# Optimization experiments

Measured on AMD Instinct MI355X. Metric: run time of the kernel, lower is better.

Reference implementation:

```python
import jax, jax.numpy as jnp
import numpy as np

N, E, CIN, COUT = 50000, 800000, 64, 64
K_MAIN, K_SC = 5, 1
EPS = 1e-15      # PyG GMMConv sigma epsilon
BN_EPS = 1e-5    # BatchNorm epsilon


def gmm_conv(x, src, dst, pseudo, g, mu, sigma, root, bias):
    """PyG GMMConv with aggr='mean', root_weight=True, bias=True.
    x: [N,Cin], pseudo: [E,dim], g: [Cin,K*Cout], mu/sigma: [K,dim],
    root: [Cin,Cout], bias: [Cout]."""
    K = mu.shape[0]
    Cout = root.shape[1]
    n = x.shape[0]
    # Gaussian mixture weights per edge: [E,K]
    diff = pseudo[:, None, :] - mu[None, :, :]                     # [E,K,dim]
    gauss = jnp.exp((-0.5 * diff * diff / (EPS + sigma[None] ** 2)).sum(-1))
    # Project node features once at node level, then gather per edge
    xp = (x @ g).reshape(n, K, Cout)                               # [N,K,Cout]
    msg = jnp.einsum('ek,ekc->ec', gauss, xp[src])                 # [E,Cout]
    agg = jax.ops.segment_sum(msg, dst, num_segments=n)            # [N,Cout]
    deg = jax.ops.segment_sum(jnp.ones((src.shape[0],), x.dtype), dst,
                              num_segments=n)
    agg = agg / jnp.clip(deg, 1.0)[:, None]                        # mean aggr
    return agg + x @ root + bias


def batch_norm(x, gamma, beta):
    # SyncBatchNorm in training mode: batch stats over the node dimension
    m = x.mean(0)
    v = x.var(0)  # biased variance, as torch uses for normalization
    return (x - m) * jax.lax.rsqrt(v + BN_EPS) * gamma + beta


def _gmm_params(key, cin, cout, k):
    k1, k2, k3, k4 = jax.random.split(key, 4)
    scale = 1.0 / np.sqrt(cin)
    g = jax.random.normal(k1, (cin, k * cout), jnp.float32) * scale
    mu = jax.random.uniform(k2, (k, 1), jnp.float32)
    sigma = 1.0 + 0.1 * jax.random.uniform(k3, (k, 1), jnp.float32)
    root = jax.random.normal(k4, (cin, cout), jnp.float32) * scale
    bias = jnp.zeros((cout,), jnp.float32)
    return g, mu, sigma, root, bias


def setup_inputs() -> dict:
    key = jax.random.key(0)
    ks = jax.random.split(key, 8)
    x = jax.random.normal(ks[0], (N, CIN), jnp.float32)
    edge_index = jax.random.randint(ks[1], (2, E), 0, N, jnp.int64)
    edge_attr = jax.random.uniform(ks[2], (E, 1), jnp.float32)
    g1, mu1, sig1, root1, b1 = _gmm_params(ks[3], CIN, COUT, K_MAIN)
    g2, mu2, sig2, root2, b2 = _gmm_params(ks[4], COUT, COUT, K_MAIN)
    gs, mus, sigs, roots, bs = _gmm_params(ks[5], CIN, COUT, K_SC)
    ones = jnp.ones((COUT,), jnp.float32)
    zeros = jnp.zeros((COUT,), jnp.float32)
    return {
        'x': x, 'edge_index': edge_index, 'edge_attr': edge_attr,
        'g1': g1, 'mu1': mu1, 'sig1': sig1, 'root1': root1, 'b1': b1,
        'gam1': ones, 'bet1': zeros,
        'g2': g2, 'mu2': mu2, 'sig2': sig2, 'root2': root2, 'b2': b2,
        'gam2': ones, 'bet2': zeros,
        'gs': gs, 'mus': mus, 'sigs': sigs, 'roots': roots, 'bs': bs,
        'gams': ones, 'bets': zeros,
    }


def reference(x, edge_index, edge_attr,
              g1, mu1, sig1, root1, b1, gam1, bet1,
              g2, mu2, sig2, root2, b2, gam2, bet2,
              gs, mus, sigs, roots, bs, gams, bets):
    src, dst = edge_index[0], edge_index[1]
    h = gmm_conv(x, src, dst, edge_attr, g1, mu1, sig1, root1, b1)
    h = jax.nn.elu(batch_norm(h, gam1, bet1))
    h = gmm_conv(h, src, dst, edge_attr, g2, mu2, sig2, root2, b2)
    h = batch_norm(h, gam2, bet2)
    sc = gmm_conv(x, src, dst, edge_attr, gs, mus, sigs, roots, bs)
    sc = batch_norm(sc, gams, bets)
    return jax.nn.elu(h + sc)
```

## Files before the change

### kernel.cpp

```cpp
#include <hip/hip_runtime.h>
#include <hip/hip_bf16.h>


#define EPS_SIGMA 1e-15f
#define BN_EPS    1e-5f
#define PAD       48

typedef unsigned short ushortT;
typedef unsigned int uintT;
typedef __attribute__((ext_vector_type(8))) short bf16x8;
typedef __attribute__((ext_vector_type(4))) float f32x4;
typedef __attribute__((ext_vector_type(2))) float f32x2;

__device__ __forceinline__ ushortT f2bf(float f) {
  uintT b = __float_as_uint(f);
  b += 0x7FFFu + ((b >> 16) & 1u);
  return (ushortT)(b >> 16);
}
__device__ __forceinline__ float bf2f(ushortT u) {
  return __uint_as_float(((uintT)u) << 16);
}
__device__ __forceinline__ uintT pk2(float a, float b) {
  return (uintT)f2bf(a) | ((uintT)f2bf(b) << 16);
}

__device__ __forceinline__ void prep_one(const float* __restrict__ g,
                                         const float* __restrict__ root,
                                         ushortT* __restrict__ Bm, int K, int t) {
  int ks = t >> 8, rem = t & 255;
  int nt = rem >> 6, lane = rem & 63;
  int kbase = ks * 32 + (lane >> 4) * 8;
  int col = nt * 16 + (lane & 15);
  ushortT o[8];
#pragma unroll
  for (int j = 0; j < 8; ++j) {
    int r = kbase + j;
    float v;
    if (r < K * 64) {
      int k = r >> 6, i = r & 63;
      v = g[(size_t)i * (K * 64) + k * 64 + col];
    } else {
      v = root[(size_t)(r - K * 64) * 64 + col];
    }
    o[j] = f2bf(v);
  }
  *(uint4*)&Bm[(size_t)t * 8] = *(const uint4*)o;
}

__global__ void prologue(const float* __restrict__ x, ushortT* __restrict__ x_bf,
                         int total, int* __restrict__ cnt, float* __restrict__ stats,
                         int n, const void* ei, int* flag,
                         const float* g1, const float* root1, ushortT* Bm1,
                         const float* g2, const float* root2, ushortT* Bm2,
                         const float* gs, const float* roots, ushortT* Bmsc) {
  int t = blockIdx.x * 256 + threadIdx.x;
  int idx = t * 4;
  if (idx + 3 < total) {
    float4 v = *(const float4*)&x[idx];
    ushortT o[4] = {f2bf(v.x), f2bf(v.y), f2bf(v.z), f2bf(v.w)};
    *(uint2*)&x_bf[idx] = *(const uint2*)o;
  }
  if (t < n) cnt[t] = 0;
  if (t < 12 * 64) stats[t] = 0.f;
  if (blockIdx.x < 12) prep_one(g1, root1, Bm1, 5, t);
  else if (blockIdx.x < 24) prep_one(g2, root2, Bm2, 5, t - 12 * 256);
  else if (blockIdx.x < 28) prep_one(gs, roots, Bmsc, 1, t - 24 * 256);
  else if (blockIdx.x == 28) {
    const int* p = (const int*)ei;
    __shared__ int bad;
    if (threadIdx.x == 0) bad = 0;
    __syncthreads();
    if (p[threadIdx.x * 2 + 1] != 0) atomicAdd(&bad, 1);
    __syncthreads();
    if (threadIdx.x == 0) *flag = (bad == 0);
  }
}

__device__ __forceinline__ int load_idx(const void* ei, size_t pos, int is64) {
  if (is64) return (int)((const long long*)ei)[pos];
  return ((const int*)ei)[pos];
}

__global__ __launch_bounds__(256) void scatter_wgt(
    const void* ei, const float* __restrict__ ea, int E, const int* flag,
    int* __restrict__ cnt,
    const float* __restrict__ mu1, const float* __restrict__ sig1,
    const float* __restrict__ mus, const float* __restrict__ sigs,
    const float* __restrict__ mu2, const float* __restrict__ sig2,
    uint4* __restrict__ wbufC) {
  int e = blockIdx.x * 256 + threadIdx.x;
  if (e >= E) return;
  int is64 = *flag;
  int s = load_idx(ei, (size_t)e, is64);
  int d = load_idx(ei, (size_t)E + e, is64);
  float p = ea[e];
  int pos = atomicAdd(&cnt[d], 1);
  float w1[6], w2[5];
#pragma unroll
  for (int k = 0; k < 5; ++k) {
    float sg = sig1[k], df = p - mu1[k];
    w1[k] = __expf(-0.5f / (EPS_SIGMA + sg * sg) * df * df);
  }
  {
    float sg = sigs[0], df = p - mus[0];
    w1[5] = __expf(-0.5f / (EPS_SIGMA + sg * sg) * df * df);
  }
#pragma unroll
  for (int k = 0; k < 5; ++k) {
    float sg = sig2[k], df = p - mu2[k];
    w2[k] = __expf(-0.5f / (EPS_SIGMA + sg * sg) * df * df);
  }
  if (pos < PAD) {
    size_t slot = (size_t)d * PAD + pos;
    wbufC[slot * 2 + 0] = make_uint4(pk2(w1[0], w1[1]), pk2(w1[2], w1[3]),
                                     pk2(w1[4], w1[5]), (uintT)s);
    wbufC[slot * 2 + 1] = make_uint4(pk2(w2[0], w2[1]), pk2(w2[2], w2[3]),
                                     pk2(w2[4], 0.f), (uintT)s);
  }
}

template <int KT>
__device__ __forceinline__ void q_fma(f32x2* acc, uint4 r, uint2 xv) {
  f32x2 xlo, xhi;
  xlo.x = bf2f((ushortT)(xv.x & 0xffffu));
  xlo.y = bf2f((ushortT)(xv.x >> 16));
  xhi.x = bf2f((ushortT)(xv.y & 0xffffu));
  xhi.y = bf2f((ushortT)(xv.y >> 16));
  float w;
  f32x2 wv;
  w = bf2f((ushortT)(r.x & 0xffffu));
  wv.x = w; wv.y = w;
  acc[0] = __builtin_elementwise_fma(wv, xlo, acc[0]);
  acc[1] = __builtin_elementwise_fma(wv, xhi, acc[1]);
  if (KT > 1) {
    w = bf2f((ushortT)(r.x >> 16));
    wv.x = w; wv.y = w;
    acc[2] = __builtin_elementwise_fma(wv, xlo, acc[2]);
    acc[3] = __builtin_elementwise_fma(wv, xhi, acc[3]);
  }
  if (KT > 2) {
    w = bf2f((ushortT)(r.y & 0xffffu));
    wv.x = w; wv.y = w;
    acc[4] = __builtin_elementwise_fma(wv, xlo, acc[4]);
    acc[5] = __builtin_elementwise_fma(wv, xhi, acc[5]);
  }
  if (KT > 3) {
    w = bf2f((ushortT)(r.y >> 16));
    wv.x = w; wv.y = w;
    acc[6] = __builtin_elementwise_fma(wv, xlo, acc[6]);
    acc[7] = __builtin_elementwise_fma(wv, xhi, acc[7]);
  }
  if (KT > 4) {
    w = bf2f((ushortT)(r.z & 0xffffu));
    wv.x = w; wv.y = w;
    acc[8] = __builtin_elementwise_fma(wv, xlo, acc[8]);
    acc[9] = __builtin_elementwise_fma(wv, xhi, acc[9]);
  }
  if (KT > 5) {
    w = bf2f((ushortT)(r.z >> 16));
    wv.x = w; wv.y = w;
    acc[10] = __builtin_elementwise_fma(wv, xlo, acc[10]);
    acc[11] = __builtin_elementwise_fma(wv, xhi, acc[11]);
  }
}

template <int KT>
__global__ __launch_bounds__(256) void agg_pre(const ushortT* __restrict__ feat,
                                               const int* __restrict__ cnt,
                                               const uint4* __restrict__ wbufC, int off,
                                               ushortT* __restrict__ out, int n, int ldo) {
  int lane = threadIdx.x & 63;
  int q = lane >> 4;
  int c4 = lane & 15;
  int node = (blockIdx.x * 4 + (threadIdx.x >> 6)) * 4 + q;
  bool act = node < n;
  int deg = act ? cnt[node] : 0;
  int cap = deg < PAD ? deg : PAD;
  int beg = node * PAD;
  int end = beg + cap;
  f32x2 acc[2 * KT];
#pragma unroll
  for (int k = 0; k < 2 * KT; ++k) acc[k] = (f32x2){0.f, 0.f};
  int i = beg;
  for (; i + 4 <= end; i += 4) {
    uint4 r0 = wbufC[(size_t)(i + 0) * 2 + off];
    uint4 r1 = wbufC[(size_t)(i + 1) * 2 + off];
    uint4 r2 = wbufC[(size_t)(i + 2) * 2 + off];
    uint4 r3 = wbufC[(size_t)(i + 3) * 2 + off];
    uint2 x0 = *(const uint2*)&feat[((size_t)r0.w << 6) + c4 * 4];
    uint2 x1 = *(const uint2*)&feat[((size_t)r1.w << 6) + c4 * 4];
    uint2 x2 = *(const uint2*)&feat[((size_t)r2.w << 6) + c4 * 4];
    uint2 x3 = *(const uint2*)&feat[((size_t)r3.w << 6) + c4 * 4];
    q_fma<KT>(acc, r0, x0);
    q_fma<KT>(acc, r1, x1);
    q_fma<KT>(acc, r2, x2);
    q_fma<KT>(acc, r3, x3);
  }
  for (; i < end; ++i) {
    uint4 r = wbufC[(size_t)i * 2 + off];
    uint2 xv = *(const uint2*)&feat[((size_t)r.w << 6) + c4 * 4];
    q_fma<KT>(acc, r, xv);
  }
  if (act) {
    float invdeg = 1.0f / (float)(deg > 1 ? deg : 1);
    uintT* outu = (uintT*)out;
    size_t obase = ((size_t)node * ldo) >> 1;
#pragma unroll
    for (int k = 0; k < KT; ++k) {
      uint2 ov = make_uint2(pk2(acc[2 * k].x * invdeg, acc[2 * k].y * invdeg),
                            pk2(acc[2 * k + 1].x * invdeg, acc[2 * k + 1].y * invdeg));
      *(uint2*)&outu[obase + k * 32 + c4 * 2] = ov;
    }
  }
}

__device__ __forceinline__ void bn_epilogue(float cs[4], float cq[4], int wid, int lane,
                                            int tid, float red_s[4][64], float red_q[4][64],
                                            float* sums, float* sumsq) {
#pragma unroll
  for (int nt = 0; nt < 4; ++nt) {
    cs[nt] += __shfl_xor(cs[nt], 16);
    cs[nt] += __shfl_xor(cs[nt], 32);
    cq[nt] += __shfl_xor(cq[nt], 16);
    cq[nt] += __shfl_xor(cq[nt], 32);
  }
  if (lane < 16) {
#pragma unroll
    for (int nt = 0; nt < 4; ++nt) {
      red_s[wid][nt * 16 + lane] = cs[nt];
      red_q[wid][nt * 16 + lane] = cq[nt];
    }
  }
  __syncthreads();
  if (tid < 64) {
    float ts = red_s[0][tid] + red_s[1][tid] + red_s[2][tid] + red_s[3][tid];
    float tq = red_q[0][tid] + red_q[1][tid] + red_q[2][tid] + red_q[3][tid];
    atomicAdd(&sums[tid], ts);
    atomicAdd(&sumsq[tid], tq);
  }
  __syncthreads();
}

__global__ __launch_bounds__(256) void gemm_mfma(const ushortT* __restrict__ A1, int lda1,
                                                 int K1, const ushortT* __restrict__ A2,
                                                 const ushortT* __restrict__ Bm,
                                                 const float* __restrict__ bias,
                                                 ushortT* __restrict__ C, int M,
                                                 float* sums, float* sumsq) {
  __shared__ float red_s[4][64];
  __shared__ float red_q[4][64];
  int tid = threadIdx.x;
  int wid = tid >> 6, lane = tid & 63;
  int row16 = lane & 15, kg = lane >> 4;
  int rowbase = blockIdx.x * 64 + wid * 16;
  int arow = rowbase + row16;
  if (arow >= M) arow = M - 1;
  const ushortT* a1p = A1 + (size_t)arow * lda1 + kg * 8;
  const ushortT* a2p = A2 + (size_t)arow * 64 + kg * 8;
  int nks1 = K1 >> 5;
  int nks = (K1 + 64) >> 5;
  f32x4 acc[4];
#pragma unroll
  for (int nt = 0; nt < 4; ++nt) acc[nt] = (f32x4){0.f, 0.f, 0.f, 0.f};
  for (int ks = 0; ks < nks; ++ks) {
    const ushortT* ap = (ks < nks1) ? (a1p + ks * 32) : (a2p + (ks - nks1) * 32);
    bf16x8 af = *(const bf16x8*)ap;
#pragma unroll
    for (int nt = 0; nt < 4; ++nt) {
      bf16x8 bfr = *(const bf16x8*)(Bm + (size_t)ks * 2048 + nt * 512 + lane * 8);
      acc[nt] = __builtin_amdgcn_mfma_f32_16x16x32_bf16(af, bfr, acc[nt], 0, 0, 0);
    }
  }
  float bv[4];
#pragma unroll
  for (int nt = 0; nt < 4; ++nt) bv[nt] = bias[nt * 16 + row16];
  float cs[4] = {}, cq[4] = {};
#pragma unroll
  for (int r = 0; r < 4; ++r) {
    int orow = rowbase + kg * 4 + r;
    if (orow < M) {
#pragma unroll
      for (int nt = 0; nt < 4; ++nt) {
        float v = acc[nt][r] + bv[nt];
        C[(size_t)orow * 64 + nt * 16 + row16] = f2bf(v);
        cs[nt] += v;
        cq[nt] = fmaf(v, v, cq[nt]);
      }
    }
  }
  bn_epilogue(cs, cq, wid, lane, tid, red_s, red_q, sums, sumsq);
}

__global__ __launch_bounds__(256) void gemm_mfma_dual(
    const ushortT* __restrict__ Abuf, const ushortT* __restrict__ X,
    const ushortT* __restrict__ Bm1, const ushortT* __restrict__ Bmsc,
    const float* __restrict__ b1, const float* __restrict__ bs,
    ushortT* __restrict__ H, ushortT* __restrict__ S, int M,
    float* sumH, float* sqH, float* sumS, float* sqS) {
  __shared__ float red_s[4][64];
  __shared__ float red_q[4][64];
  int tid = threadIdx.x;
  int wid = tid >> 6, lane = tid & 63;
  int row16 = lane & 15, kg = lane >> 4;
  int rowbase = blockIdx.x * 64 + wid * 16;
  int arow = rowbase + row16;
  if (arow >= M) arow = M - 1;
  const ushortT* ab = Abuf + (size_t)arow * 384 + kg * 8;
  const ushortT* xb = X + (size_t)arow * 64 + kg * 8;
  f32x4 accH[4], accS[4];
#pragma unroll
  for (int nt = 0; nt < 4; ++nt) {
    accH[nt] = (f32x4){0.f, 0.f, 0.f, 0.f};
    accS[nt] = (f32x4){0.f, 0.f, 0.f, 0.f};
  }
  for (int ks = 0; ks < 10; ++ks) {
    bf16x8 af = *(const bf16x8*)(ab + ks * 32);
#pragma unroll
    for (int nt = 0; nt < 4; ++nt) {
      bf16x8 bfr = *(const bf16x8*)(Bm1 + (size_t)ks * 2048 + nt * 512 + lane * 8);
      accH[nt] = __builtin_amdgcn_mfma_f32_16x16x32_bf16(af, bfr, accH[nt], 0, 0, 0);
    }
  }
#pragma unroll
  for (int ks = 0; ks < 2; ++ks) {
    bf16x8 af = *(const bf16x8*)(ab + 320 + ks * 32);
#pragma unroll
    for (int nt = 0; nt < 4; ++nt) {
      bf16x8 bfr = *(const bf16x8*)(Bmsc + (size_t)ks * 2048 + nt * 512 + lane * 8);
      accS[nt] = __builtin_amdgcn_mfma_f32_16x16x32_bf16(af, bfr, accS[nt], 0, 0, 0);
    }
  }
#pragma unroll
  for (int ks = 0; ks < 2; ++ks) {
    bf16x8 af = *(const bf16x8*)(xb + ks * 32);
#pragma unroll
    for (int nt = 0; nt < 4; ++nt) {
      bf16x8 bfrH = *(const bf16x8*)(Bm1 + (size_t)(10 + ks) * 2048 + nt * 512 + lane * 8);
      accH[nt] = __builtin_amdgcn_mfma_f32_16x16x32_bf16(af, bfrH, accH[nt], 0, 0, 0);
      bf16x8 bfrS = *(const bf16x8*)(Bmsc + (size_t)(2 + ks) * 2048 + nt * 512 + lane * 8);
      accS[nt] = __builtin_amdgcn_mfma_f32_16x16x32_bf16(af, bfrS, accS[nt], 0, 0, 0);
    }
  }
  float bvH[4], bvS[4];
#pragma unroll
  for (int nt = 0; nt < 4; ++nt) {
    bvH[nt] = b1[nt * 16 + row16];
    bvS[nt] = bs[nt * 16 + row16];
  }
  float csH[4] = {}, cqH[4] = {}, csS[4] = {}, cqS[4] = {};
#pragma unroll
  for (int r = 0; r < 4; ++r) {
    int orow = rowbase + kg * 4 + r;
    if (orow < M) {
#pragma unroll
      for (int nt = 0; nt < 4; ++nt) {
        float vh = accH[nt][r] + bvH[nt];
        float vs = accS[nt][r] + bvS[nt];
        H[(size_t)orow * 64 + nt * 16 + row16] = f2bf(vh);
        S[(size_t)orow * 64 + nt * 16 + row16] = f2bf(vs);
        csH[nt] += vh;
        cqH[nt] = fmaf(vh, vh, cqH[nt]);
        csS[nt] += vs;
        cqS[nt] = fmaf(vs, vs, cqS[nt]);
      }
    }
  }
  bn_epilogue(csH, cqH, wid, lane, tid, red_s, red_q, sumH, sqH);
  bn_epilogue(csS, cqS, wid, lane, tid, red_s, red_q, sumS, sqS);
}

__global__ void norm_elu(const ushortT* __restrict__ Hbf, ushortT* __restrict__ h_bf,
                         const float* __restrict__ stats, const float* __restrict__ gam,
                         const float* __restrict__ bet, float inv_n, int total4) {
  __shared__ float sc_s[64], sh_s[64];
  int tid = threadIdx.x;
  if (tid < 64) {
    float m = stats[tid] * inv_n;
    float v = stats[64 + tid] * inv_n - m * m;
    float r = rsqrtf(v + BN_EPS);
    float s = r * gam[tid];
    sc_s[tid] = s;
    sh_s[tid] = bet[tid] - m * s;
  }
  __syncthreads();
  int t = blockIdx.x * 256 + tid;
  if (t >= total4) return;
  int idx = t * 4;
  int c = idx & 63;
  uint2 hv = *(const uint2*)&Hbf[idx];
  float v0 = bf2f((ushortT)(hv.x & 0xffffu)) * sc_s[c] + sh_s[c];
  float v1 = bf2f((ushortT)(hv.x >> 16)) * sc_s[c + 1] + sh_s[c + 1];
  float v2 = bf2f((ushortT)(hv.y & 0xffffu)) * sc_s[c + 2] + sh_s[c + 2];
  float v3 = bf2f((ushortT)(hv.y >> 16)) * sc_s[c + 3] + sh_s[c + 3];
  v0 = v0 > 0.f ? v0 : expm1f(v0);
  v1 = v1 > 0.f ? v1 : expm1f(v1);
  v2 = v2 > 0.f ? v2 : expm1f(v2);
  v3 = v3 > 0.f ? v3 : expm1f(v3);
  *(uint2*)&h_bf[idx] = make_uint2(pk2(v0, v1), pk2(v2, v3));
}

__global__ void final_kernel(const ushortT* __restrict__ h2, const ushortT* __restrict__ scb,
                             const float* __restrict__ stats,
                             const float* __restrict__ gam2, const float* __restrict__ bet2,
                             const float* __restrict__ gams, const float* __restrict__ bets,
                             float inv_n, float* __restrict__ out, int total4) {
  __shared__ float s2_s[64], t2_s[64], ss_s[64], ts_s[64];
  int tid = threadIdx.x;
  if (tid < 64) {
    float m = stats[2 * 64 + tid] * inv_n;
    float v = stats[3 * 64 + tid] * inv_n - m * m;
    float r = rsqrtf(v + BN_EPS);
    float s = r * gam2[tid];
    s2_s[tid] = s;
    t2_s[tid] = bet2[tid] - m * s;
  } else if (tid < 128) {
    int c = tid - 64;
    float m = stats[4 * 64 + c] * inv_n;
    float v = stats[5 * 64 + c] * inv_n - m * m;
    float r = rsqrtf(v + BN_EPS);
    float s = r * gams[c];
    ss_s[c] = s;
    ts_s[c] = bets[c] - m * s;
  }
  __syncthreads();
  int t = blockIdx.x * 256 + tid;
  if (t >= total4) return;
  int idx = t * 4;
  int c = idx & 63;
  uint2 hv = *(const uint2*)&h2[idx];
  uint2 sv = *(const uint2*)&scb[idx];
  float v0 = bf2f((ushortT)(hv.x & 0xffffu)) * s2_s[c] + t2_s[c] +
             bf2f((ushortT)(sv.x & 0xffffu)) * ss_s[c] + ts_s[c];
  float v1 = bf2f((ushortT)(hv.x >> 16)) * s2_s[c + 1] + t2_s[c + 1] +
             bf2f((ushortT)(sv.x >> 16)) * ss_s[c + 1] + ts_s[c + 1];
  float v2 = bf2f((ushortT)(hv.y & 0xffffu)) * s2_s[c + 2] + t2_s[c + 2] +
             bf2f((ushortT)(sv.y & 0xffffu)) * ss_s[c + 2] + ts_s[c + 2];
  float v3 = bf2f((ushortT)(hv.y >> 16)) * s2_s[c + 3] + t2_s[c + 3] +
             bf2f((ushortT)(sv.y >> 16)) * ss_s[c + 3] + ts_s[c + 3];
  float4 o;
  o.x = v0 > 0.f ? v0 : expm1f(v0);
  o.y = v1 > 0.f ? v1 : expm1f(v1);
  o.z = v2 > 0.f ? v2 : expm1f(v2);
  o.w = v3 > 0.f ? v3 : expm1f(v3);
  *(float4*)&out[idx] = o;
}

extern "C" void kernel_launch(void* const* d_in, const int* in_sizes, int n_in,
                              void* d_out, int out_size, void* d_ws, size_t ws_size,
                              hipStream_t stream) {
  const float* x    = (const float*)d_in[0];
  const void*  ei   = d_in[1];
  const float* ea   = (const float*)d_in[2];
  const float* g1   = (const float*)d_in[3];
  const float* mu1  = (const float*)d_in[4];
  const float* sig1 = (const float*)d_in[5];
  const float* root1= (const float*)d_in[6];
  const float* b1   = (const float*)d_in[7];
  const float* gam1 = (const float*)d_in[8];
  const float* bet1 = (const float*)d_in[9];
  const float* g2   = (const float*)d_in[10];
  const float* mu2  = (const float*)d_in[11];
  const float* sig2 = (const float*)d_in[12];
  const float* root2= (const float*)d_in[13];
  const float* b2   = (const float*)d_in[14];
  const float* gam2 = (const float*)d_in[15];
  const float* bet2 = (const float*)d_in[16];
  const float* gs   = (const float*)d_in[17];
  const float* mus  = (const float*)d_in[18];
  const float* sigs = (const float*)d_in[19];
  const float* roots= (const float*)d_in[20];
  const float* bs   = (const float*)d_in[21];
  const float* gams = (const float*)d_in[22];
  const float* bets = (const float*)d_in[23];

  int N = in_sizes[0] / 64;
  int E = in_sizes[1] / 2;

  char* w = (char*)d_ws;
  auto alloc = [&](size_t bytes) {
    char* p = w;
    w += (bytes + 255) & ~(size_t)255;
    return p;
  };
  int*     flag    = (int*)alloc(256);
  int*     cnt     = (int*)alloc((size_t)N * 4);
  uint4*   wbufC   = (uint4*)alloc((size_t)N * PAD * 32);
  ushortT* Abuf    = (ushortT*)alloc((size_t)N * 384 * 2);
  ushortT* x_bf    = (ushortT*)alloc((size_t)N * 64 * 2);
  ushortT* h_bf    = (ushortT*)alloc((size_t)N * 64 * 2);
  ushortT* Hpre    = (ushortT*)alloc((size_t)N * 64 * 2);
  ushortT* scb     = (ushortT*)alloc((size_t)N * 64 * 2);
  ushortT* Bm1     = (ushortT*)alloc(12 * 2048 * 2);
  ushortT* Bm2     = (ushortT*)alloc(12 * 2048 * 2);
  ushortT* Bmsc    = (ushortT*)alloc(4 * 2048 * 2);
  float*   stats   = (float*)alloc(12 * 64 * 4);
  ushortT* h2b = (ushortT*)wbufC;

  int eb = (E + 255) / 256;
  int total4 = (N * 64) / 4;
  int nb_e4 = (total4 + 255) / 256;
  float inv_n = 1.0f / (float)N;

  prologue<<<nb_e4, 256, 0, stream>>>(x, x_bf, N * 64, cnt, stats, N, ei, flag,
                                      g1, root1, Bm1, g2, root2, Bm2, gs, roots, Bmsc);

  scatter_wgt<<<eb, 256, 0, stream>>>(ei, ea, E, flag, cnt,
                                      mu1, sig1, mus, sigs, mu2, sig2, wbufC);

  int mtiles = (N + 63) / 64;
  int nb_node16 = (N + 15) / 16;

  agg_pre<6><<<nb_node16, 256, 0, stream>>>(x_bf, cnt, wbufC, 0, Abuf, N, 384);
  gemm_mfma_dual<<<mtiles, 256, 0, stream>>>(Abuf, x_bf, Bm1, Bmsc, b1, bs, Hpre, scb, N,
                                             stats + 0 * 64, stats + 1 * 64,
                                             stats + 4 * 64, stats + 5 * 64);
  norm_elu<<<nb_e4, 256, 0, stream>>>(Hpre, h_bf, stats, gam1, bet1, inv_n, total4);

  agg_pre<5><<<nb_node16, 256, 0, stream>>>(h_bf, cnt, wbufC, 1, Abuf, N, 320);
  gemm_mfma<<<mtiles, 256, 0, stream>>>(Abuf, 320, 320, h_bf, Bm2, b2, h2b, N,
                                        stats + 2 * 64, stats + 3 * 64);

  final_kernel<<<nb_e4, 256, 0, stream>>>(h2b, scb, stats, gam2, bet2, gams, bets,
                                          inv_n, (float*)d_out, total4);
}
```

Baseline: 186.9 us.

## Store raw edge attribute per slot and compute Gaussian weights inside aggregation

```diff
diff --git a/kernel.cpp b/kernel.cpp
--- a/kernel.cpp
+++ b/kernel.cpp
@@ -81,13 +81,9 @@
   return ((const int*)ei)[pos];
 }
 
-__global__ __launch_bounds__(256) void scatter_wgt(
+__global__ __launch_bounds__(256) void scatter_edge(
     const void* ei, const float* __restrict__ ea, int E, const int* flag,
-    int* __restrict__ cnt,
-    const float* __restrict__ mu1, const float* __restrict__ sig1,
-    const float* __restrict__ mus, const float* __restrict__ sigs,
-    const float* __restrict__ mu2, const float* __restrict__ sig2,
-    uint4* __restrict__ wbufC) {
+    int* __restrict__ cnt, uint2* __restrict__ wrec) {
   int e = blockIdx.x * 256 + threadIdx.x;
   if (e >= E) return;
   int is64 = *flag;
@@ -95,80 +91,50 @@
   int d = load_idx(ei, (size_t)E + e, is64);
   float p = ea[e];
   int pos = atomicAdd(&cnt[d], 1);
-  float w1[6], w2[5];
-#pragma unroll
-  for (int k = 0; k < 5; ++k) {
-    float sg = sig1[k], df = p - mu1[k];
-    w1[k] = __expf(-0.5f / (EPS_SIGMA + sg * sg) * df * df);
-  }
-  {
-    float sg = sigs[0], df = p - mus[0];
-    w1[5] = __expf(-0.5f / (EPS_SIGMA + sg * sg) * df * df);
-  }
-#pragma unroll
-  for (int k = 0; k < 5; ++k) {
-    float sg = sig2[k], df = p - mu2[k];
-    w2[k] = __expf(-0.5f / (EPS_SIGMA + sg * sg) * df * df);
-  }
   if (pos < PAD) {
-    size_t slot = (size_t)d * PAD + pos;
-    wbufC[slot * 2 + 0] = make_uint4(pk2(w1[0], w1[1]), pk2(w1[2], w1[3]),
-                                     pk2(w1[4], w1[5]), (uintT)s);
-    wbufC[slot * 2 + 1] = make_uint4(pk2(w2[0], w2[1]), pk2(w2[2], w2[3]),
-                                     pk2(w2[4], 0.f), (uintT)s);
+    wrec[(size_t)d * PAD + pos] = make_uint2(__float_as_uint(p), (uintT)s);
   }
 }
 
 template <int KT>
-__device__ __forceinline__ void q_fma(f32x2* acc, uint4 r, uint2 xv) {
+__device__ __forceinline__ void q_fma2(f32x2* acc, const float* w, uint2 xv) {
   f32x2 xlo, xhi;
   xlo.x = bf2f((ushortT)(xv.x & 0xffffu));
   xlo.y = bf2f((ushortT)(xv.x >> 16));
   xhi.x = bf2f((ushortT)(xv.y & 0xffffu));
   xhi.y = bf2f((ushortT)(xv.y >> 16));
-  float w;
-  f32x2 wv;
-  w = bf2f((ushortT)(r.x & 0xffffu));
-  wv.x = w; wv.y = w;
-  acc[0] = __builtin_elementwise_fma(wv, xlo, acc[0]);
-  acc[1] = __builtin_elementwise_fma(wv, xhi, acc[1]);
-  if (KT > 1) {
-    w = bf2f((ushortT)(r.x >> 16));
-    wv.x = w; wv.y = w;
-    acc[2] = __builtin_elementwise_fma(wv, xlo, acc[2]);
-    acc[3] = __builtin_elementwise_fma(wv, xhi, acc[3]);
-  }
-  if (KT > 2) {
-    w = bf2f((ushortT)(r.y & 0xffffu));
-    wv.x = w; wv.y = w;
-    acc[4] = __builtin_elementwise_fma(wv, xlo, acc[4]);
-    acc[5] = __builtin_elementwise_fma(wv, xhi, acc[5]);
-  }
-  if (KT > 3) {
-    w = bf2f((ushortT)(r.y >> 16));
-    wv.x = w; wv.y = w;
-    acc[6] = __builtin_elementwise_fma(wv, xlo, acc[6]);
-    acc[7] = __builtin_elementwise_fma(wv, xhi, acc[7]);
-  }
-  if (KT > 4) {
-    w = bf2f((ushortT)(r.z & 0xffffu));
-    wv.x = w; wv.y = w;
-    acc[8] = __builtin_elementwise_fma(wv, xlo, acc[8]);
-    acc[9] = __builtin_elementwise_fma(wv, xhi, acc[9]);
-  }
-  if (KT > 5) {
-    w = bf2f((ushortT)(r.z >> 16));
-    wv.x = w; wv.y = w;
-    acc[10] = __builtin_elementwise_fma(wv, xlo, acc[10]);
-    acc[11] = __builtin_elementwise_fma(wv, xhi, acc[11]);
-  }
-}
-
-template <int KT>
+#pragma unroll
+  for (int k = 0; k < KT; ++k) {
+    f32x2 wv;
+    wv.x = w[k]; wv.y = w[k];
+    acc[2 * k]     = __builtin_elementwise_fma(wv, xlo, acc[2 * k]);
+    acc[2 * k + 1] = __builtin_elementwise_fma(wv, xhi, acc[2 * k + 1]);
+  }
+}
+
+template <int KA, int KB>
 __global__ __launch_bounds__(256) void agg_pre(const ushortT* __restrict__ feat,
                                                const int* __restrict__ cnt,
-                                               const uint4* __restrict__ wbufC, int off,
+                                               const uint2* __restrict__ wrec,
+                                               const float* __restrict__ muA,
+                                               const float* __restrict__ sigA,
+                                               const float* __restrict__ muB,
+                                               const float* __restrict__ sigB,
                                                ushortT* __restrict__ out, int n, int ldo) {
+  const int KT = KA + KB;
+  float mk[KT], ck[KT];
+#pragma unroll
+  for (int k = 0; k < KA; ++k) {
+    mk[k] = muA[k];
+    float sg = sigA[k];
+    ck[k] = -0.5f / (EPS_SIGMA + sg * sg);
+  }
+#pragma unroll
+  for (int k = 0; k < KB; ++k) {
+    mk[KA + k] = muB[k];
+    float sg = sigB[k];
+    ck[KA + k] = -0.5f / (EPS_SIGMA + sg * sg);
+  }
   int lane = threadIdx.x & 63;
   int q = lane >> 4;
   int c4 = lane & 15;
@@ -183,23 +149,43 @@
   for (int k = 0; k < 2 * KT; ++k) acc[k] = (f32x2){0.f, 0.f};
   int i = beg;
   for (; i + 4 <= end; i += 4) {
-    uint4 r0 = wbufC[(size_t)(i + 0) * 2 + off];
-    uint4 r1 = wbufC[(size_t)(i + 1) * 2 + off];
-    uint4 r2 = wbufC[(size_t)(i + 2) * 2 + off];
-    uint4 r3 = wbufC[(size_t)(i + 3) * 2 + off];
-    uint2 x0 = *(const uint2*)&feat[((size_t)r0.w << 6) + c4 * 4];
-    uint2 x1 = *(const uint2*)&feat[((size_t)r1.w << 6) + c4 * 4];
-    uint2 x2 = *(const uint2*)&feat[((size_t)r2.w << 6) + c4 * 4];
-    uint2 x3 = *(const uint2*)&feat[((size_t)r3.w << 6) + c4 * 4];
-    q_fma<KT>(acc, r0, x0);
-    q_fma<KT>(acc, r1, x1);
-    q_fma<KT>(acc, r2, x2);
-    q_fma<KT>(acc, r3, x3);
+    uint2 r0 = wrec[i + 0];
+    uint2 r1 = wrec[i + 1];
+    uint2 r2 = wrec[i + 2];
+    uint2 r3 = wrec[i + 3];
+    uint2 x0 = *(const uint2*)&feat[((size_t)r0.y << 6) + c4 * 4];
+    uint2 x1 = *(const uint2*)&feat[((size_t)r1.y << 6) + c4 * 4];
+    uint2 x2 = *(const uint2*)&feat[((size_t)r2.y << 6) + c4 * 4];
+    uint2 x3 = *(const uint2*)&feat[((size_t)r3.y << 6) + c4 * 4];
+    float p0 = __uint_as_float(r0.x);
+    float p1 = __uint_as_float(r1.x);
+    float p2 = __uint_as_float(r2.x);
+    float p3 = __uint_as_float(r3.x);
+    float w0[KT], w1[KT], w2[KT], w3[KT];
+#pragma unroll
+    for (int k = 0; k < KT; ++k) {
+      float d0 = p0 - mk[k], d1 = p1 - mk[k], d2 = p2 - mk[k], d3 = p3 - mk[k];
+      w0[k] = __expf(ck[k] * d0 * d0);
+      w1[k] = __expf(ck[k] * d1 * d1);
+      w2[k] = __expf(ck[k] * d2 * d2);
+      w3[k] = __expf(ck[k] * d3 * d3);
+    }
+    q_fma2<KT>(acc, w0, x0);
+    q_fma2<KT>(acc, w1, x1);
+    q_fma2<KT>(acc, w2, x2);
+    q_fma2<KT>(acc, w3, x3);
   }
   for (; i < end; ++i) {
-    uint4 r = wbufC[(size_t)i * 2 + off];
-    uint2 xv = *(const uint2*)&feat[((size_t)r.w << 6) + c4 * 4];
-    q_fma<KT>(acc, r, xv);
+    uint2 r = wrec[i];
+    uint2 xv = *(const uint2*)&feat[((size_t)r.y << 6) + c4 * 4];
+    float p = __uint_as_float(r.x);
+    float w[KT];
+#pragma unroll
+    for (int k = 0; k < KT; ++k) {
+      float df = p - mk[k];
+      w[k] = __expf(ck[k] * df * df);
+    }
+    q_fma2<KT>(acc, w, xv);
   }
   if (act) {
     float invdeg = 1.0f / (float)(deg > 1 ? deg : 1);
@@ -484,17 +470,17 @@
   };
   int*     flag    = (int*)alloc(256);
   int*     cnt     = (int*)alloc((size_t)N * 4);
-  uint4*   wbufC   = (uint4*)alloc((size_t)N * PAD * 32);
+  uint2*   wrec    = (uint2*)alloc((size_t)N * PAD * 8);
   ushortT* Abuf    = (ushortT*)alloc((size_t)N * 384 * 2);
   ushortT* x_bf    = (ushortT*)alloc((size_t)N * 64 * 2);
   ushortT* h_bf    = (ushortT*)alloc((size_t)N * 64 * 2);
   ushortT* Hpre    = (ushortT*)alloc((size_t)N * 64 * 2);
   ushortT* scb     = (ushortT*)alloc((size_t)N * 64 * 2);
+  ushortT* h2b     = (ushortT*)alloc((size_t)N * 64 * 2);
   ushortT* Bm1     = (ushortT*)alloc(12 * 2048 * 2);
   ushortT* Bm2     = (ushortT*)alloc(12 * 2048 * 2);
   ushortT* Bmsc    = (ushortT*)alloc(4 * 2048 * 2);
   float*   stats   = (float*)alloc(12 * 64 * 4);
-  ushortT* h2b = (ushortT*)wbufC;
 
   int eb = (E + 255) / 256;
   int total4 = (N * 64) / 4;
@@ -504,19 +490,20 @@
   prologue<<<nb_e4, 256, 0, stream>>>(x, x_bf, N * 64, cnt, stats, N, ei, flag,
                                       g1, root1, Bm1, g2, root2, Bm2, gs, roots, Bmsc);
 
-  scatter_wgt<<<eb, 256, 0, stream>>>(ei, ea, E, flag, cnt,
-                                      mu1, sig1, mus, sigs, mu2, sig2, wbufC);
+  scatter_edge<<<eb, 256, 0, stream>>>(ei, ea, E, flag, cnt, wrec);
 
   int mtiles = (N + 63) / 64;
   int nb_node16 = (N + 15) / 16;
 
-  agg_pre<6><<<nb_node16, 256, 0, stream>>>(x_bf, cnt, wbufC, 0, Abuf, N, 384);
+  agg_pre<5, 1><<<nb_node16, 256, 0, stream>>>(x_bf, cnt, wrec, mu1, sig1, mus, sigs,
+                                               Abuf, N, 384);
   gemm_mfma_dual<<<mtiles, 256, 0, stream>>>(Abuf, x_bf, Bm1, Bmsc, b1, bs, Hpre, scb, N,
                                              stats + 0 * 64, stats + 1 * 64,
                                              stats + 4 * 64, stats + 5 * 64);
   norm_elu<<<nb_e4, 256, 0, stream>>>(Hpre, h_bf, stats, gam1, bet1, inv_n, total4);
 
-  agg_pre<5><<<nb_node16, 256, 0, stream>>>(h_bf, cnt, wbufC, 1, Abuf, N, 320);
+  agg_pre<5, 0><<<nb_node16, 256, 0, stream>>>(h_bf, cnt, wrec, mu2, sig2, nullptr, nullptr,
+                                               Abuf, N, 320);
   gemm_mfma<<<mtiles, 256, 0, stream>>>(Abuf, 320, 320, h_bf, Bm2, b2, h2b, N,
                                         stats + 2 * 64, stats + 3 * 64);
 
```

After: 203.5 us. +8.9%, slower.
